# Optimization experiments

Measured on AMD Instinct MI355X. Metric: run time of the kernel, lower is better.

## Reference

```python
import jax, jax.numpy as jnp
import numpy as np

L = 6      # num encoder / decoder layers
H = 8      # num heads
D = 512    # dim_word
FF = 2048  # dim_feedforward
B = 8
S = 512


def _linear(x, W, b):
    return x @ W + b


def _mha(x_q, x_kv, W, b, num_heads):
    # W: [4, D, D] (q, k, v, out) stored as [in, out]; b: [4, D]
    Bb, Tq, Dd = x_q.shape
    Tk = x_kv.shape[1]
    dh = Dd // num_heads
    q = _linear(x_q, W[0], b[0]).reshape(Bb, Tq, num_heads, dh)
    k = _linear(x_kv, W[1], b[1]).reshape(Bb, Tk, num_heads, dh)
    v = _linear(x_kv, W[2], b[2]).reshape(Bb, Tk, num_heads, dh)
    # NOTE: original code divides by sqrt(dim_key_query_ALL_heads) == sqrt(D),
    # not sqrt(per-head dim) -- faithful to source.
    scores = jnp.einsum('bqhd,bkhd->bhqk', q, k) / jnp.sqrt(jnp.asarray(Dd, q.dtype))
    p = jax.nn.softmax(scores, axis=-1)
    z = jnp.einsum('bhqk,bkhd->bqhd', p, v).reshape(Bb, Tq, Dd)
    return _linear(z, W[3], b[3])


def _ln(z, alpha, beta):
    # Source uses torch .std() => unbiased (ddof=1), and NO epsilon.
    mean = jnp.mean(z, axis=-1, keepdims=True)
    std = jnp.std(z, axis=-1, ddof=1, keepdims=True)
    return (z - mean) / std * alpha + beta


def _ffn(x, W1, b1, W2, b2):
    return _linear(jax.nn.relu(_linear(x, W1, b1)), W2, b2)


def _forward(input_encoder, input_decoder, enc_W, enc_b, enc_W1, enc_b1,
             enc_W2, enc_b2, enc_alpha, enc_beta, dec_W, dec_b, dec_W1,
             dec_b1, dec_W2, dec_b2, dec_alpha, dec_beta, final_alpha,
             final_beta):
    z = input_encoder
    for i in range(L):
        a = _mha(z, z, enc_W[i], enc_b[i], H)
        z = _ln(a + z, enc_alpha[i, 0], enc_beta[i, 0])
        f = _ffn(z, enc_W1[i], enc_b1[i], enc_W2[i], enc_b2[i])
        z = _ln(z + f, enc_alpha[i, 1], enc_beta[i, 1])
    z_enc = _ln(z, final_alpha[0], final_beta[0])

    z = input_decoder
    for i in range(L):
        a = _mha(z, z, dec_W[i, 0], dec_b[i, 0], H)
        z1 = _ln(a + z, dec_alpha[i, 0], dec_beta[i, 0])
        c = _mha(z1, z_enc, dec_W[i, 1], dec_b[i, 1], H)
        z2 = _ln(c + z1, dec_alpha[i, 1], dec_beta[i, 1])
        f = _ffn(z2, dec_W1[i], dec_b1[i], dec_W2[i], dec_b2[i])
        z = _ln(z2 + f, dec_alpha[i, 2], dec_beta[i, 2])
    return _ln(z, final_alpha[1], final_beta[1])


def setup_inputs() -> dict:
    key = jax.random.key(0)
    ks = jax.random.split(key, 12)
    w_scale = 1.0 / np.sqrt(D)
    inp = {
        'input_encoder': jax.random.normal(ks[0], (B, S, D), jnp.float32),
        'input_decoder': jax.random.normal(ks[1], (B, S, D), jnp.float32),
        'enc_W': jax.random.normal(ks[2], (L, 4, D, D), jnp.float32) * w_scale,
        'enc_b': jnp.zeros((L, 4, D), jnp.float32),
        'enc_W1': jax.random.normal(ks[3], (L, D, FF), jnp.float32) * w_scale,
        'enc_b1': jnp.zeros((L, FF), jnp.float32),
        'enc_W2': jax.random.normal(ks[4], (L, FF, D), jnp.float32) * (1.0 / np.sqrt(FF)),
        'enc_b2': jnp.zeros((L, D), jnp.float32),
        'enc_alpha': jnp.ones((L, 2, D), jnp.float32),
        'enc_beta': jnp.zeros((L, 2, D), jnp.float32),
        'dec_W': jax.random.normal(ks[5], (L, 2, 4, D, D), jnp.float32) * w_scale,
        'dec_b': jnp.zeros((L, 2, 4, D), jnp.float32),
        'dec_W1': jax.random.normal(ks[6], (L, D, FF), jnp.float32) * w_scale,
        'dec_b1': jnp.zeros((L, FF), jnp.float32),
        'dec_W2': jax.random.normal(ks[7], (L, FF, D), jnp.float32) * (1.0 / np.sqrt(FF)),
        'dec_b2': jnp.zeros((L, D), jnp.float32),
        'dec_alpha': jnp.ones((L, 3, D), jnp.float32),
        'dec_beta': jnp.zeros((L, 3, D), jnp.float32),
        'final_alpha': jnp.ones((2, D), jnp.float32),
        'final_beta': jnp.zeros((2, D), jnp.float32),
    }
    return inp


def reference(input_encoder, input_decoder, enc_W, enc_b, enc_W1, enc_b1,
              enc_W2, enc_b2, enc_alpha, enc_beta, dec_W, dec_b, dec_W1,
              dec_b1, dec_W2, dec_b2, dec_alpha, dec_beta, final_alpha,
              final_beta):
    return _forward(input_encoder, input_decoder, enc_W, enc_b, enc_W1,
                    enc_b1, enc_W2, enc_b2, enc_alpha, enc_beta, dec_W,
                    dec_b, dec_W1, dec_b1, dec_W2, dec_b2, dec_alpha,
                    dec_beta, final_alpha, final_beta)
```

## Files before the change

### kernel.cpp

```cpp
#include <hip/hip_runtime.h>
#include <hip/hip_bf16.h>
#include <cstdint>

using bf16 = __hip_bfloat16;

typedef __bf16 bf16x8_t __attribute__((ext_vector_type(8)));
typedef float f32x4_t __attribute__((ext_vector_type(4)));
typedef unsigned short u16x8 __attribute__((ext_vector_type(8)));

enum { EPI_BF16 = 0, EPI_QKV = 2, EPI_RELU = 4 };

__device__ __forceinline__ unsigned short f2bf_bits(float f) {
    bf16 h = __float2bfloat16(f);
    return *reinterpret_cast<unsigned short*>(&h);
}
__device__ __forceinline__ float bfbits2f(unsigned short u) {
    return __uint_as_float(((unsigned)u) << 16);
}
__device__ __forceinline__ void gload16(const void* g, void* l) {
    __builtin_amdgcn_global_load_lds(
        (const __attribute__((address_space(1))) void*)g,
        (__attribute__((address_space(3))) void*)l, 16, 0, 0);
}

__global__ __launch_bounds__(256) void wtrans_kernel(
    const float* __restrict__ W, bf16* __restrict__ Wt, int Kd, int Nd) {
    __shared__ float tile[32][33];
    const int b = blockIdx.z;
    const float* Wb = W + (size_t)b * Kd * Nd;
    bf16* Tb = Wt + (size_t)b * Kd * Nd;
    const int n0 = blockIdx.x * 32, k0 = blockIdx.y * 32;
    const int tx = threadIdx.x, ty = threadIdx.y;
#pragma unroll
    for (int i = 0; i < 32; i += 8)
        tile[ty + i][tx] = Wb[(size_t)(k0 + ty + i) * Nd + n0 + tx];
    __syncthreads();
#pragma unroll
    for (int i = 0; i < 32; i += 8)
        Tb[(size_t)(n0 + ty + i) * Kd + k0 + tx] = __float2bfloat16(tile[tx][ty + i]);
}

__global__ __launch_bounds__(256) void dualcast_kernel(
    const float* __restrict__ x, float* __restrict__ of, bf16* __restrict__ ob) {
    const int i = blockIdx.x * 256 + threadIdx.x;
    float4 v = ((const float4*)x)[i];
    ((float4*)of)[i] = v;
    uint2 pk;
    pk.x = ((unsigned)f2bf_bits(v.y) << 16) | f2bf_bits(v.x);
    pk.y = ((unsigned)f2bf_bits(v.w) << 16) | f2bf_bits(v.z);
    ((uint2*)ob)[i] = pk;
}

template <int BM, int BN, int EPI, bool HASBIAS, int NT = 256, int WM = 2, int WN = 2>
__global__ __launch_bounds__(NT) void gemm_nt(
    const bf16* __restrict__ A, const bf16* __restrict__ B,
    const float* __restrict__ bias, void* __restrict__ Cout, void* __restrict__ Caux,
    int K, int ldA, int ldB, int ldC, int vcol0,
    long long oBz, long long oCz, long long oCvz, long long oBiasz) {
    static_assert(BM % 32 == 0 && BN % 32 == 0, "tile");
    static_assert(WM * WN == NT / 64, "wave grid");
    constexpr int RR = NT / 8;
    static_assert(BM % RR == 0 && BN % RR == 0, "staging");
    constexpr int WTM = (BM / WM) / 16;
    constexpr int WTN = (BN / WN) / 16;
    __shared__ alignas(16) bf16 lsA0[BM * 64];
    __shared__ alignas(16) bf16 lsB0[BN * 64];
    __shared__ alignas(16) bf16 lsA1[BM * 64];
    __shared__ alignas(16) bf16 lsB1[BN * 64];

    const int t = threadIdx.x;
    const int lane = t & 63;
    const int wave = t >> 6;
    const int wm = wave / WN, wn = wave % WN;
    const int z = blockIdx.z;

    const int brow = blockIdx.x * BM, bcol = blockIdx.y * BN;
    const bf16* Ab = A + (size_t)brow * ldA;
    const bf16* Bb = B + (long long)z * oBz + (size_t)bcol * ldB;
    const float* biasz = HASBIAS ? bias + (long long)z * oBiasz : bias;

    const int srow = t >> 3;
    const int sdst = (t & 7) * 8;
    const int ssrc = ((t & 7) ^ (srow & 7)) * 8;

    f32x4_t acc[WTM][WTN] = {};

#define GEMM_STAGE(AA, BB, kt)                                                \
    {                                                                         \
        _Pragma("unroll")                                                     \
        for (int r = 0; r < BM / RR; ++r)                                     \
            gload16(Ab + (size_t)(srow + r * RR) * ldA + (kt) + ssrc,         \
                    &AA[(srow + r * RR) * 64 + sdst]);                        \
        _Pragma("unroll")                                                     \
        for (int r = 0; r < BN / RR; ++r)                                     \
            gload16(Bb + (size_t)(srow + r * RR) * ldB + (kt) + ssrc,         \
                    &BB[(srow + r * RR) * 64 + sdst]);                        \
    }

#define GEMM_COMPUTE(AA, BB)                                                  \
    {                                                                         \
        _Pragma("unroll")                                                     \
        for (int ks = 0; ks < 2; ++ks) {                                      \
            bf16x8_t af[WTM], bfr[WTN];                                       \
            _Pragma("unroll")                                                 \
            for (int m = 0; m < WTM; ++m) {                                   \
                const int rowA = wm * (BM / WM) + m * 16 + (lane & 15);       \
                const int slot = ks * 4 + (lane >> 4);                        \
                af[m] = *(const bf16x8_t*)&AA[rowA * 64 + ((slot ^ (rowA & 7)) * 8)]; \
            }                                                                 \
            _Pragma("unroll")                                                 \
            for (int n = 0; n < WTN; ++n) {                                   \
                const int rowB = wn * (BN / WN) + n * 16 + (lane & 15);       \
                const int slot = ks * 4 + (lane >> 4);                        \
                bfr[n] = *(const bf16x8_t*)&BB[rowB * 64 + ((slot ^ (rowB & 7)) * 8)]; \
            }                                                                 \
            _Pragma("unroll")                                                 \
            for (int m = 0; m < WTM; ++m)                                     \
                _Pragma("unroll")                                             \
                for (int n = 0; n < WTN; ++n)                                 \
                    acc[m][n] = __builtin_amdgcn_mfma_f32_16x16x32_bf16(      \
                        af[m], bfr[n], acc[m][n], 0, 0, 0);                   \
        }                                                                     \
    }

    GEMM_STAGE(lsA0, lsB0, 0);
    __syncthreads();
    int kt = 0;
    while (true) {
        int kn = kt + 64;
        if (kn < K) GEMM_STAGE(lsA1, lsB1, kn);
        GEMM_COMPUTE(lsA0, lsB0);
        __syncthreads();
        kt = kn;
        if (kt >= K) break;
        kn = kt + 64;
        if (kn < K) GEMM_STAGE(lsA0, lsB0, kn);
        GEMM_COMPUTE(lsA1, lsB1);
        __syncthreads();
        kt = kn;
        if (kt >= K) break;
    }
#undef GEMM_STAGE
#undef GEMM_COMPUTE

    const int lr = (lane >> 4) * 4, lc = lane & 15;
#pragma unroll
    for (int m = 0; m < WTM; ++m) {
        const int gr0 = brow + wm * (BM / WM) + m * 16 + lr;
#pragma unroll
        for (int n = 0; n < WTN; ++n) {
            const int gc = bcol + wn * (BN / WN) + n * 16 + lc;
            float bv = 0.f;
            if constexpr (HASBIAS) bv = biasz[gc];
            float v[4];
#pragma unroll
            for (int r = 0; r < 4; ++r) {
                float x = acc[m][n][r] + bv;
                if constexpr (EPI == EPI_RELU) x = fmaxf(x, 0.f);
                v[r] = x;
            }
            if constexpr (EPI == EPI_QKV) {
                if (gc >= vcol0) {
                    bf16* Cv = (bf16*)Caux + (long long)z * oCvz;
                    const int bb = gr0 >> 9, q = gr0 & 511;
                    union { unsigned short h[4]; uint2 u; } pk;
#pragma unroll
                    for (int r = 0; r < 4; ++r) pk.h[r] = f2bf_bits(v[r]);
                    *(uint2*)&Cv[(size_t)bb * 262144 + (size_t)(gc - vcol0) * 512 + q] = pk.u;
                } else {
                    bf16* C = (bf16*)Cout + (long long)z * oCz;
#pragma unroll
                    for (int r = 0; r < 4; ++r)
                        C[(size_t)(gr0 + r) * ldC + gc] = __float2bfloat16(v[r]);
                }
            } else {
                bf16* C = (bf16*)Cout + (long long)z * oCz;
#pragma unroll
                for (int r = 0; r < 4; ++r)
                    C[(size_t)(gr0 + r) * ldC + gc] = __float2bfloat16(v[r]);
            }
        }
    }
}

__global__ __launch_bounds__(256) void flash_kernel(
    const bf16* __restrict__ Q, const bf16* __restrict__ Kg,
    const bf16* __restrict__ Vt, bf16* __restrict__ O,
    int ldK, int ldO, float qscale) {
    __shared__ alignas(16) bf16 klds[128 * 64];
    __shared__ alignas(16) bf16 vlds[64 * 128];
    __shared__ alignas(16) unsigned short plds[4][16 * 136];

    const int t = threadIdx.x, lane = t & 63, w = t >> 6;
    const int bh = blockIdx.x;
    const int b = bh >> 3, h = bh & 7;
    const int qb = blockIdx.y;

    const bf16* Qb = Q + (size_t)(b * 512 + qb * 64) * 1024 + h * 64;
    const bf16* Kb = Kg + (size_t)(b * 512) * ldK + h * 64;
    const bf16* Vb = Vt + (size_t)b * 262144 + (size_t)(h * 64) * 512;

    bf16x8_t qf[2];
    {
        const bf16* qr = Qb + (size_t)(w * 16 + (lane & 15)) * 1024 + (lane >> 4) * 8;
        qf[0] = *(const bf16x8_t*)qr;
        qf[1] = *(const bf16x8_t*)(qr + 32);
    }

    f32x4_t oacc[4] = {};
    float mrow[4] = {-1e30f, -1e30f, -1e30f, -1e30f};
    float lrow[4] = {0.f, 0.f, 0.f, 0.f};

    for (int kt = 0; kt < 4; ++kt) {
#pragma unroll
        for (int rd = 0; rd < 4; ++rd) {
            const int id = t + rd * 256;
            const int kr = id >> 3, sl = id & 7;
            gload16(Kb + (size_t)(kt * 128 + kr) * ldK + ((sl ^ (kr & 7)) * 8),
                    &klds[id * 8]);
        }
#pragma unroll
        for (int rd = 0; rd < 4; ++rd) {
            const int id = t + rd * 256;
            const int dr = id >> 4, sl = id & 15;
            gload16(Vb + (size_t)dr * 512 + kt * 128 + ((sl ^ (dr & 7)) * 8),
                    &vlds[id * 8]);
        }
        __syncthreads();

        f32x4_t sc[8] = {};
        __builtin_amdgcn_s_setprio(1);
#pragma unroll
        for (int kf = 0; kf < 8; ++kf) {
            const int krow = kf * 16 + (lane & 15);
#pragma unroll
            for (int ks = 0; ks < 2; ++ks) {
                const int slot = (ks * 4 + (lane >> 4)) ^ (krow & 7);
                bf16x8_t kfr = *(const bf16x8_t*)&klds[krow * 64 + slot * 8];
                sc[kf] = __builtin_amdgcn_mfma_f32_16x16x32_bf16(qf[ks], kfr, sc[kf], 0, 0, 0);
            }
        }
        __builtin_amdgcn_s_setprio(0);
        float tm[4] = {-1e30f, -1e30f, -1e30f, -1e30f};
#pragma unroll
        for (int kf = 0; kf < 8; ++kf)
#pragma unroll
            for (int r = 0; r < 4; ++r) {
                sc[kf][r] *= qscale;
                tm[r] = fmaxf(tm[r], sc[kf][r]);
            }
#pragma unroll
        for (int mm = 1; mm < 16; mm <<= 1)
#pragma unroll
            for (int r = 0; r < 4; ++r) tm[r] = fmaxf(tm[r], __shfl_xor(tm[r], mm, 64));
        float mnew[4], scal[4], ts[4] = {0.f, 0.f, 0.f, 0.f};
#pragma unroll
        for (int r = 0; r < 4; ++r) {
            mnew[r] = fmaxf(mrow[r], tm[r]);
            scal[r] = __expf(mrow[r] - mnew[r]);
            mrow[r] = mnew[r];
        }
#pragma unroll
        for (int kf = 0; kf < 8; ++kf)
#pragma unroll
            for (int r = 0; r < 4; ++r) {
                const float p = __expf(sc[kf][r] - mnew[r]);
                ts[r] += p;
                plds[w][((lane >> 4) * 4 + r) * 136 + kf * 16 + (lane & 15)] = f2bf_bits(p);
            }
#pragma unroll
        for (int mm = 1; mm < 16; mm <<= 1)
#pragma unroll
            for (int r = 0; r < 4; ++r) ts[r] += __shfl_xor(ts[r], mm, 64);
#pragma unroll
        for (int r = 0; r < 4; ++r) lrow[r] = lrow[r] * scal[r] + ts[r];
#pragma unroll
        for (int n = 0; n < 4; ++n)
#pragma unroll
            for (int r = 0; r < 4; ++r) oacc[n][r] *= scal[r];
        __builtin_amdgcn_s_setprio(1);
#pragma unroll
        for (int ks2 = 0; ks2 < 4; ++ks2) {
            bf16x8_t pa =
                *(const bf16x8_t*)&plds[w][(lane & 15) * 136 + ks2 * 32 + (lane >> 4) * 8];
#pragma unroll
            for (int n = 0; n < 4; ++n) {
                const int drow = n * 16 + (lane & 15);
                const int slot = (ks2 * 4 + (lane >> 4)) ^ (drow & 7);
                bf16x8_t vbf = *(const bf16x8_t*)&vlds[drow * 128 + slot * 8];
                oacc[n] = __builtin_amdgcn_mfma_f32_16x16x32_bf16(pa, vbf, oacc[n], 0, 0, 0);
            }
        }
        __builtin_amdgcn_s_setprio(0);
        __syncthreads();
    }
    bf16* Ob = O + (size_t)(b * 512 + qb * 64 + w * 16) * ldO + h * 64;
#pragma unroll
    for (int r = 0; r < 4; ++r) {
        const float inv = 1.0f / lrow[r];
        bf16* orow = Ob + (size_t)((lane >> 4) * 4 + r) * ldO;
#pragma unroll
        for (int n = 0; n < 4; ++n)
            orow[n * 16 + (lane & 15)] = __float2bfloat16(oacc[n][r] * inv);
    }
}

__global__ __launch_bounds__(256) void add_ln_kernel(
    const bf16* __restrict__ a, const float* __restrict__ x,
    const float* __restrict__ alpha, const float* __restrict__ beta,
    float* __restrict__ of, bf16* __restrict__ ob) {
    const int row = blockIdx.x * 4 + (threadIdx.x >> 6);
    const int lane = threadIdx.x & 63;
    const size_t base = (size_t)row * 512 + lane * 8;
    float v[8];
    {
        const float4* xp = (const float4*)(x + base);
        float4 x0 = xp[0], x1 = xp[1];
        v[0] = x0.x; v[1] = x0.y; v[2] = x0.z; v[3] = x0.w;
        v[4] = x1.x; v[5] = x1.y; v[6] = x1.z; v[7] = x1.w;
    }
    if (a) {
        u16x8 u = *(const u16x8*)(a + base);
#pragma unroll
        for (int j = 0; j < 8; ++j) v[j] += bfbits2f(u[j]);
    }
    float s = 0.f, ss = 0.f;
#pragma unroll
    for (int j = 0; j < 8; ++j) { s += v[j]; ss += v[j] * v[j]; }
#pragma unroll
    for (int m = 1; m < 64; m <<= 1) {
        s += __shfl_xor(s, m, 64);
        ss += __shfl_xor(ss, m, 64);
    }
    const float mean = s * (1.0f / 512.0f);
    const float var = (ss - s * mean) * (1.0f / 511.0f);
    const float rstd = rsqrtf(var);
    const int col = lane * 8;
    const float4* alp = (const float4*)(alpha + col);
    const float4* bep = (const float4*)(beta + col);
    float4 al0 = alp[0], al1 = alp[1], be0 = bep[0], be1 = bep[1];
    float al[8] = {al0.x, al0.y, al0.z, al0.w, al1.x, al1.y, al1.z, al1.w};
    float be[8] = {be0.x, be0.y, be0.z, be0.w, be1.x, be1.y, be1.z, be1.w};
    float y[8];
#pragma unroll
    for (int j = 0; j < 8; ++j) y[j] = (v[j] - mean) * rstd * al[j] + be[j];
    if (of) {
        float4 o0, o1;
        o0.x = y[0]; o0.y = y[1]; o0.z = y[2]; o0.w = y[3];
        o1.x = y[4]; o1.y = y[5]; o1.z = y[6]; o1.w = y[7];
        float4* op = (float4*)(of + base);
        op[0] = o0; op[1] = o1;
    }
    if (ob) {
        u16x8 u;
#pragma unroll
        for (int j = 0; j < 8; ++j) u[j] = f2bf_bits(y[j]);
        *(u16x8*)(ob + base) = u;
    }
}

extern "C" void kernel_launch(void* const* d_in, const int* in_sizes, int n_in,
                              void* d_out, int out_size, void* d_ws, size_t ws_size,
                              hipStream_t stream) {
    (void)in_sizes; (void)n_in; (void)out_size;

    const float* in_enc = (const float*)d_in[0];
    const float* in_dec = (const float*)d_in[1];
    const float* enc_W  = (const float*)d_in[2];
    const float* enc_b  = (const float*)d_in[3];
    const float* enc_W1 = (const float*)d_in[4];
    const float* enc_b1 = (const float*)d_in[5];
    const float* enc_W2 = (const float*)d_in[6];
    const float* enc_b2 = (const float*)d_in[7];
    const float* enc_al = (const float*)d_in[8];
    const float* enc_be = (const float*)d_in[9];
    const float* dec_W  = (const float*)d_in[10];
    const float* dec_b  = (const float*)d_in[11];
    const float* dec_W1 = (const float*)d_in[12];
    const float* dec_b1 = (const float*)d_in[13];
    const float* dec_W2 = (const float*)d_in[14];
    const float* dec_b2 = (const float*)d_in[15];
    const float* dec_al = (const float*)d_in[16];
    const float* dec_be = (const float*)d_in[17];
    const float* fin_al = (const float*)d_in[18];
    const float* fin_be = (const float*)d_in[19];

    constexpr int Dm = 512, FFm = 2048, Lm = 6;
    constexpr int M = 4096;
    const size_t DD = (size_t)Dm * Dm;
    const size_t DFF = (size_t)Dm * FFm;
    const long long MD = (long long)M * Dm;
    const float QSCALE = 0.04419417382415922f;

    char* wsp = (char*)d_ws;
    auto alloc = [&](size_t bytes) -> char* {
        char* p = wsp;
        wsp += (bytes + 255) & ~(size_t)255;
        return p;
    };

    bf16* wtEncW  = (bf16*)alloc(sizeof(bf16) * 24 * DD);
    bf16* wtEncW1 = (bf16*)alloc(sizeof(bf16) * 6 * DFF);
    bf16* wtEncW2 = (bf16*)alloc(sizeof(bf16) * 6 * DFF);
    bf16* wtDecW  = (bf16*)alloc(sizeof(bf16) * 48 * DD);
    bf16* wtDecW1 = (bf16*)alloc(sizeof(bf16) * 6 * DFF);
    bf16* wtDecW2 = (bf16*)alloc(sizeof(bf16) * 6 * DFF);
    bf16* qkvbuf = (bf16*)alloc(sizeof(bf16) * M * 1024);
    bf16* vt     = (bf16*)alloc(sizeof(bf16) * M * Dm);
    bf16* ckbuf  = (bf16*)alloc(sizeof(bf16) * M * Dm);
    bf16* ck6    = (bf16*)alloc(sizeof(bf16) * 6 * M * Dm);
    bf16* cv6    = (bf16*)alloc(sizeof(bf16) * 6 * M * Dm);
    bf16* ffnmid = (bf16*)alloc(sizeof(bf16) * M * FFm);
    bf16* projb  = (bf16*)alloc(sizeof(bf16) * M * Dm);
    float* zAf = (float*)alloc(sizeof(float) * M * Dm);
    bf16*  zAb = (bf16*)alloc(sizeof(bf16) * M * Dm);
    float* zBf = (float*)alloc(sizeof(float) * M * Dm);
    bf16*  zBb = (bf16*)alloc(sizeof(bf16) * M * Dm);
    bf16*  zencb = (bf16*)alloc(sizeof(bf16) * M * Dm);

    if ((size_t)(wsp - (char*)d_ws) > ws_size) return;

    {
        dim3 bl(32, 8);
        wtrans_kernel<<<dim3(Dm / 32, Dm / 32, 24), bl, 0, stream>>>(enc_W, wtEncW, Dm, Dm);
        wtrans_kernel<<<dim3(FFm / 32, Dm / 32, 6), bl, 0, stream>>>(enc_W1, wtEncW1, Dm, FFm);
        wtrans_kernel<<<dim3(Dm / 32, FFm / 32, 6), bl, 0, stream>>>(enc_W2, wtEncW2, FFm, Dm);
        wtrans_kernel<<<dim3(Dm / 32, Dm / 32, 48), bl, 0, stream>>>(dec_W, wtDecW, Dm, Dm);
        wtrans_kernel<<<dim3(FFm / 32, Dm / 32, 6), bl, 0, stream>>>(dec_W1, wtDecW1, Dm, FFm);
        wtrans_kernel<<<dim3(Dm / 32, FFm / 32, 6), bl, 0, stream>>>(dec_W2, wtDecW2, FFm, Dm);
    }

    float* curF = zAf; bf16* curB = zAb;
    float* othF = zBf; bf16* othB = zBb;
    auto swapbuf = [&]() {
        float* tf = curF; curF = othF; othF = tf;
        bf16* tb = curB; curB = othB; othB = tb;
    };

    auto self_attention = [&](const bf16* src, const bf16* Wt4, const float* b4) {
        gemm_nt<128, 128, EPI_QKV, true, 512, 2, 4><<<dim3(32, 12, 1), 512, 0, stream>>>(
            src, Wt4, b4, qkvbuf, vt, Dm, Dm, Dm, 1024, 1024, 0, 0, 0, 0);
        flash_kernel<<<dim3(64, 8), 256, 0, stream>>>(
            qkvbuf, qkvbuf + 512, vt, ckbuf, 1024, 512, QSCALE);
        gemm_nt<64, 64, EPI_BF16, true, 256, 2, 2><<<dim3(64, 8, 1), 256, 0, stream>>>(
            ckbuf, Wt4 + 3 * DD, b4 + 3 * Dm, projb, nullptr, Dm, 512, Dm, Dm, 0,
            0, 0, 0, 0);
    };

    auto cross_attention = [&](const bf16* src, const bf16* Wt4, const float* b4, int i) {
        gemm_nt<64, 64, EPI_BF16, true, 256, 2, 2><<<dim3(64, 8, 1), 256, 0, stream>>>(
            src, Wt4, b4, qkvbuf, nullptr, Dm, Dm, Dm, 1024, 0, 0, 0, 0, 0);
        flash_kernel<<<dim3(64, 8), 256, 0, stream>>>(
            qkvbuf, ck6 + (long long)i * MD, cv6 + (long long)i * MD, qkvbuf + 512,
            512, 1024, QSCALE);
        gemm_nt<64, 64, EPI_BF16, true, 256, 2, 2><<<dim3(64, 8, 1), 256, 0, stream>>>(
            qkvbuf + 512, Wt4 + 3 * DD, b4 + 3 * Dm, projb, nullptr, Dm, 1024, Dm, Dm, 0,
            0, 0, 0, 0);
    };

    auto ffn = [&](const bf16* src, const bf16* W1t, const float* b1v,
                   const bf16* W2t, const float* b2v) {
        gemm_nt<128, 128, EPI_RELU, true, 512, 2, 4><<<dim3(32, 16, 1), 512, 0, stream>>>(
            src, W1t, b1v, ffnmid, nullptr, Dm, Dm, Dm, FFm, 0, 0, 0, 0, 0);
        gemm_nt<64, 64, EPI_BF16, true, 256, 2, 2><<<dim3(64, 8, 1), 256, 0, stream>>>(
            ffnmid, W2t, b2v, projb, nullptr, FFm, FFm, FFm, Dm, 0, 0, 0, 0, 0);
    };

    dualcast_kernel<<<2048, 256, 0, stream>>>(in_enc, curF, curB);
    for (int i = 0; i < Lm; ++i) {
        self_attention(curB, wtEncW + (size_t)i * 4 * DD, enc_b + (size_t)i * 4 * Dm);
        add_ln_kernel<<<1024, 256, 0, stream>>>(
            projb, curF, enc_al + (size_t)(i * 2) * Dm, enc_be + (size_t)(i * 2) * Dm,
            othF, othB);
        swapbuf();
        ffn(curB, wtEncW1 + (size_t)i * DFF, enc_b1 + (size_t)i * FFm,
            wtEncW2 + (size_t)i * DFF, enc_b2 + (size_t)i * Dm);
        add_ln_kernel<<<1024, 256, 0, stream>>>(
            projb, curF, enc_al + (size_t)(i * 2 + 1) * Dm, enc_be + (size_t)(i * 2 + 1) * Dm,
            othF, othB);
        swapbuf();
    }
    add_ln_kernel<<<1024, 256, 0, stream>>>(nullptr, curF, fin_al, fin_be, nullptr, zencb);

    gemm_nt<128, 128, EPI_QKV, true, 512, 2, 4><<<dim3(32, 8, 6), 512, 0, stream>>>(
        zencb, wtDecW + 5 * DD, dec_b + 5 * Dm, ck6, cv6, Dm, Dm, Dm, 512, 512,
        8LL * (long long)DD, MD, MD, 8LL * Dm);

    curF = zAf; curB = zAb; othF = zBf; othB = zBb;
    dualcast_kernel<<<2048, 256, 0, stream>>>(in_dec, curF, curB);
    for (int i = 0; i < Lm; ++i) {
        self_attention(curB, wtDecW + (size_t)(i * 2 + 0) * 4 * DD,
                       dec_b + (size_t)(i * 2 + 0) * 4 * Dm);
        add_ln_kernel<<<1024, 256, 0, stream>>>(
            projb, curF, dec_al + (size_t)(i * 3 + 0) * Dm, dec_be + (size_t)(i * 3 + 0) * Dm,
            othF, othB);
        swapbuf();
        cross_attention(curB, wtDecW + (size_t)(i * 2 + 1) * 4 * DD,
                        dec_b + (size_t)(i * 2 + 1) * 4 * Dm, i);
        add_ln_kernel<<<1024, 256, 0, stream>>>(
            projb, curF, dec_al + (size_t)(i * 3 + 1) * Dm, dec_be + (size_t)(i * 3 + 1) * Dm,
            othF, othB);
        swapbuf();
        ffn(curB, wtDecW1 + (size_t)i * DFF, dec_b1 + (size_t)i * FFm,
            wtDecW2 + (size_t)i * DFF, dec_b2 + (size_t)i * Dm);
        add_ln_kernel<<<1024, 256, 0, stream>>>(
            projb, curF, dec_al + (size_t)(i * 3 + 2) * Dm, dec_be + (size_t)(i * 3 + 2) * Dm,
            othF, othB);
        swapbuf();
    }
    add_ln_kernel<<<1024, 256, 0, stream>>>(nullptr, curF, fin_al + Dm, fin_be + Dm,
                                            (float*)d_out, nullptr);
}
```

Before: 1.325 ms.

## Stage GEMM and attention outputs through LDS and drop fp32 residual stream

GEMM epilogues now write their tiles into a swizzled LDS buffer that aliases the staging buffers, then issue coalesced 16-byte global stores. The V-transpose path gets the same treatment, and the flash kernel output is also staged in LDS. The fp32 residual copies are removed, so add+LayerNorm reads the bf16 residual and writes only bf16. This cuts global traffic and uncoalesced stores, at the cost of an extra barrier and reduced precision on the residual stream.

Measured after the change: 1.217 ms. -8.1%, faster.

```diff
diff --git a/kernel.cpp b/kernel.cpp
--- a/kernel.cpp
+++ b/kernel.cpp
@@ -40,11 +40,10 @@
         Tb[(size_t)(n0 + ty + i) * Kd + k0 + tx] = __float2bfloat16(tile[tx][ty + i]);
 }
 
-__global__ __launch_bounds__(256) void dualcast_kernel(
-    const float* __restrict__ x, float* __restrict__ of, bf16* __restrict__ ob) {
+__global__ __launch_bounds__(256) void cast_kernel(
+    const float* __restrict__ x, bf16* __restrict__ ob) {
     const int i = blockIdx.x * 256 + threadIdx.x;
     float4 v = ((const float4*)x)[i];
-    ((float4*)of)[i] = v;
     uint2 pk;
     pk.x = ((unsigned)f2bf_bits(v.y) << 16) | f2bf_bits(v.x);
     pk.y = ((unsigned)f2bf_bits(v.w) << 16) | f2bf_bits(v.z);
@@ -63,10 +62,13 @@
     static_assert(BM % RR == 0 && BN % RR == 0, "staging");
     constexpr int WTM = (BM / WM) / 16;
     constexpr int WTN = (BN / WN) / 16;
-    __shared__ alignas(16) bf16 lsA0[BM * 64];
-    __shared__ alignas(16) bf16 lsB0[BN * 64];
-    __shared__ alignas(16) bf16 lsA1[BM * 64];
-    __shared__ alignas(16) bf16 lsB1[BN * 64];
+    constexpr int STG = 2 * (BM + BN) * 64;
+    constexpr int CTE = BM * BN;
+    __shared__ alignas(16) bf16 smem[STG > CTE ? STG : CTE];
+    bf16* lsA0 = smem;
+    bf16* lsB0 = smem + BM * 64;
+    bf16* lsA1 = smem + (BM + BN) * 64;
+    bf16* lsB1 = lsA1 + BM * 64;
 
     const int t = threadIdx.x;
     const int lane = t & 63;
@@ -144,41 +146,50 @@
 #undef GEMM_COMPUTE
 
     const int lr = (lane >> 4) * 4, lc = lane & 15;
+    const bool isV = (EPI == EPI_QKV) && (bcol >= vcol0);
+    unsigned short* cts = (unsigned short*)smem;
 #pragma unroll
     for (int m = 0; m < WTM; ++m) {
-        const int gr0 = brow + wm * (BM / WM) + m * 16 + lr;
+        const int row0 = wm * (BM / WM) + m * 16 + lr;
 #pragma unroll
         for (int n = 0; n < WTN; ++n) {
-            const int gc = bcol + wn * (BN / WN) + n * 16 + lc;
+            const int col = wn * (BN / WN) + n * 16 + lc;
             float bv = 0.f;
-            if constexpr (HASBIAS) bv = biasz[gc];
-            float v[4];
+            if constexpr (HASBIAS) bv = biasz[bcol + col];
+            unsigned short h4[4];
 #pragma unroll
             for (int r = 0; r < 4; ++r) {
                 float x = acc[m][n][r] + bv;
                 if constexpr (EPI == EPI_RELU) x = fmaxf(x, 0.f);
-                v[r] = x;
+                h4[r] = f2bf_bits(x);
             }
-            if constexpr (EPI == EPI_QKV) {
-                if (gc >= vcol0) {
-                    bf16* Cv = (bf16*)Caux + (long long)z * oCvz;
-                    const int bb = gr0 >> 9, q = gr0 & 511;
-                    union { unsigned short h[4]; uint2 u; } pk;
-#pragma unroll
-                    for (int r = 0; r < 4; ++r) pk.h[r] = f2bf_bits(v[r]);
-                    *(uint2*)&Cv[(size_t)bb * 262144 + (size_t)(gc - vcol0) * 512 + q] = pk.u;
-                } else {
-                    bf16* C = (bf16*)Cout + (long long)z * oCz;
-#pragma unroll
-                    for (int r = 0; r < 4; ++r)
-                        C[(size_t)(gr0 + r) * ldC + gc] = __float2bfloat16(v[r]);
-                }
+            if (isV) {
+                union { unsigned short h[4]; uint2 u; } pk;
+#pragma unroll
+                for (int r = 0; r < 4; ++r) pk.h[r] = h4[r];
+                *(uint2*)&cts[col * BM + (row0 ^ ((col & 7) << 3))] = pk.u;
             } else {
-                bf16* C = (bf16*)Cout + (long long)z * oCz;
 #pragma unroll
                 for (int r = 0; r < 4; ++r)
-                    C[(size_t)(gr0 + r) * ldC + gc] = __float2bfloat16(v[r]);
+                    cts[(row0 + r) * BN + (col ^ (((row0 + r) & 7) << 3))] = h4[r];
             }
+        }
+    }
+    __syncthreads();
+    if (isV) {
+        bf16* Cv = (bf16*)Caux + (long long)z * oCvz;
+        const int bb = brow >> 9, qb0 = brow & 511;
+        for (int s = t; s < CTE / 8; s += NT) {
+            const int d = s / (BM / 8), q8 = (s % (BM / 8)) * 8;
+            u16x8 val = *(const u16x8*)&cts[d * BM + (q8 ^ ((d & 7) << 3))];
+            *(u16x8*)&Cv[(size_t)bb * 262144 + (size_t)(bcol - vcol0 + d) * 512 + qb0 + q8] = val;
+        }
+    } else {
+        bf16* C = (bf16*)Cout + (long long)z * oCz;
+        for (int s = t; s < CTE / 8; s += NT) {
+            const int row = s / (BN / 8), c8 = (s % (BN / 8)) * 8;
+            u16x8 val = *(const u16x8*)&cts[row * BN + (c8 ^ ((row & 7) << 3))];
+            *(u16x8*)&C[(size_t)(brow + row) * ldC + bcol + c8] = val;
         }
     }
 }
@@ -294,19 +305,29 @@
         __builtin_amdgcn_s_setprio(0);
         __syncthreads();
     }
-    bf16* Ob = O + (size_t)(b * 512 + qb * 64 + w * 16) * ldO + h * 64;
 #pragma unroll
     for (int r = 0; r < 4; ++r) {
         const float inv = 1.0f / lrow[r];
-        bf16* orow = Ob + (size_t)((lane >> 4) * 4 + r) * ldO;
 #pragma unroll
         for (int n = 0; n < 4; ++n)
-            orow[n * 16 + (lane & 15)] = __float2bfloat16(oacc[n][r] * inv);
+            plds[w][((lane >> 4) * 4 + r) * 136 + n * 16 + (lane & 15)] =
+                f2bf_bits(oacc[n][r] * inv);
+    }
+    __syncthreads();
+    {
+        bf16* Ob = O + (size_t)(b * 512 + qb * 64 + w * 16) * ldO + h * 64;
+#pragma unroll
+        for (int it = 0; it < 2; ++it) {
+            const int seg = lane + it * 64;
+            const int row = seg >> 3, c8 = (seg & 7) * 8;
+            u16x8 val = *(const u16x8*)&plds[w][row * 136 + c8];
+            *(u16x8*)&Ob[(size_t)row * ldO + c8] = val;
+        }
     }
 }
 
 __global__ __launch_bounds__(256) void add_ln_kernel(
-    const bf16* __restrict__ a, const float* __restrict__ x,
+    const bf16* __restrict__ a, const bf16* __restrict__ x,
     const float* __restrict__ alpha, const float* __restrict__ beta,
     float* __restrict__ of, bf16* __restrict__ ob) {
     const int row = blockIdx.x * 4 + (threadIdx.x >> 6);
@@ -314,15 +335,14 @@
     const size_t base = (size_t)row * 512 + lane * 8;
     float v[8];
     {
-        const float4* xp = (const float4*)(x + base);
-        float4 x0 = xp[0], x1 = xp[1];
-        v[0] = x0.x; v[1] = x0.y; v[2] = x0.z; v[3] = x0.w;
-        v[4] = x1.x; v[5] = x1.y; v[6] = x1.z; v[7] = x1.w;
+        u16x8 ux = *(const u16x8*)(x + base);
+#pragma unroll
+        for (int j = 0; j < 8; ++j) v[j] = bfbits2f(ux[j]);
     }
     if (a) {
-        u16x8 u = *(const u16x8*)(a + base);
-#pragma unroll
-        for (int j = 0; j < 8; ++j) v[j] += bfbits2f(u[j]);
+        u16x8 ua = *(const u16x8*)(a + base);
+#pragma unroll
+        for (int j = 0; j < 8; ++j) v[j] += bfbits2f(ua[j]);
     }
     float s = 0.f, ss = 0.f;
 #pragma unroll
@@ -344,18 +364,18 @@
     float y[8];
 #pragma unroll
     for (int j = 0; j < 8; ++j) y[j] = (v[j] - mean) * rstd * al[j] + be[j];
+    if (ob) {
+        u16x8 u;
+#pragma unroll
+        for (int j = 0; j < 8; ++j) u[j] = f2bf_bits(y[j]);
+        *(u16x8*)(ob + base) = u;
+    }
     if (of) {
         float4 o0, o1;
         o0.x = y[0]; o0.y = y[1]; o0.z = y[2]; o0.w = y[3];
         o1.x = y[4]; o1.y = y[5]; o1.z = y[6]; o1.w = y[7];
         float4* op = (float4*)(of + base);
         op[0] = o0; op[1] = o1;
-    }
-    if (ob) {
-        u16x8 u;
-#pragma unroll
-        for (int j = 0; j < 8; ++j) u[j] = f2bf_bits(y[j]);
-        *(u16x8*)(ob + base) = u;
     }
 }
 
@@ -412,11 +432,9 @@
     bf16* cv6    = (bf16*)alloc(sizeof(bf16) * 6 * M * Dm);
     bf16* ffnmid = (bf16*)alloc(sizeof(bf16) * M * FFm);
     bf16* projb  = (bf16*)alloc(sizeof(bf16) * M * Dm);
-    float* zAf = (float*)alloc(sizeof(float) * M * Dm);
-    bf16*  zAb = (bf16*)alloc(sizeof(bf16) * M * Dm);
-    float* zBf = (float*)alloc(sizeof(float) * M * Dm);
-    bf16*  zBb = (bf16*)alloc(sizeof(bf16) * M * Dm);
-    bf16*  zencb = (bf16*)alloc(sizeof(bf16) * M * Dm);
+    bf16* zAb = (bf16*)alloc(sizeof(bf16) * M * Dm);
+    bf16* zBb = (bf16*)alloc(sizeof(bf16) * M * Dm);
+    bf16* zencb = (bf16*)alloc(sizeof(bf16) * M * Dm);
 
     if ((size_t)(wsp - (char*)d_ws) > ws_size) return;
 
@@ -430,12 +448,9 @@
         wtrans_kernel<<<dim3(Dm / 32, FFm / 32, 6), bl, 0, stream>>>(dec_W2, wtDecW2, FFm, Dm);
     }
 
-    float* curF = zAf; bf16* curB = zAb;
-    float* othF = zBf; bf16* othB = zBb;
-    auto swapbuf = [&]() {
-        float* tf = curF; curF = othF; othF = tf;
-        bf16* tb = curB; curB = othB; othB = tb;
-    };
+    bf16* curB = zAb;
+    bf16* othB = zBb;
+    auto swapbuf = [&]() { bf16* tb = curB; curB = othB; othB = tb; };
 
     auto self_attention = [&](const bf16* src, const bf16* Wt4, const float* b4) {
         gemm_nt<128, 128, EPI_QKV, true, 512, 2, 4><<<dim3(32, 12, 1), 512, 0, stream>>>(
@@ -466,48 +481,48 @@
             ffnmid, W2t, b2v, projb, nullptr, FFm, FFm, FFm, Dm, 0, 0, 0, 0, 0);
     };
 
-    dualcast_kernel<<<2048, 256, 0, stream>>>(in_enc, curF, curB);
+    cast_kernel<<<2048, 256, 0, stream>>>(in_enc, curB);
     for (int i = 0; i < Lm; ++i) {
         self_attention(curB, wtEncW + (size_t)i * 4 * DD, enc_b + (size_t)i * 4 * Dm);
         add_ln_kernel<<<1024, 256, 0, stream>>>(
-            projb, curF, enc_al + (size_t)(i * 2) * Dm, enc_be + (size_t)(i * 2) * Dm,
-            othF, othB);
+            projb, curB, enc_al + (size_t)(i * 2) * Dm, enc_be + (size_t)(i * 2) * Dm,
+            nullptr, othB);
         swapbuf();
         ffn(curB, wtEncW1 + (size_t)i * DFF, enc_b1 + (size_t)i * FFm,
             wtEncW2 + (size_t)i * DFF, enc_b2 + (size_t)i * Dm);
         add_ln_kernel<<<1024, 256, 0, stream>>>(
-            projb, curF, enc_al + (size_t)(i * 2 + 1) * Dm, enc_be + (size_t)(i * 2 + 1) * Dm,
-            othF, othB);
+            projb, curB, enc_al + (size_t)(i * 2 + 1) * Dm, enc_be + (size_t)(i * 2 + 1) * Dm,
+            nullptr, othB);
         swapbuf();
     }
-    add_ln_kernel<<<1024, 256, 0, stream>>>(nullptr, curF, fin_al, fin_be, nullptr, zencb);
+    add_ln_kernel<<<1024, 256, 0, stream>>>(nullptr, curB, fin_al, fin_be, nullptr, zencb);
 
     gemm_nt<128, 128, EPI_QKV, true, 512, 2, 4><<<dim3(32, 8, 6), 512, 0, stream>>>(
         zencb, wtDecW + 5 * DD, dec_b + 5 * Dm, ck6, cv6, Dm, Dm, Dm, 512, 512,
         8LL * (long long)DD, MD, MD, 8LL * Dm);
 
-    curF = zAf; curB = zAb; othF = zBf; othB = zBb;
-    dualcast_kernel<<<2048, 256, 0, stream>>>(in_dec, curF, curB);
+    curB = zAb; othB = zBb;
+    cast_kernel<<<2048, 256, 0, stream>>>(in_dec, curB);
     for (int i = 0; i < Lm; ++i) {
         self_attention(curB, wtDecW + (size_t)(i * 2 + 0) * 4 * DD,
                        dec_b + (size_t)(i * 2 + 0) * 4 * Dm);
         add_ln_kernel<<<1024, 256, 0, stream>>>(
-            projb, curF, dec_al + (size_t)(i * 3 + 0) * Dm, dec_be + (size_t)(i * 3 + 0) * Dm,
-            othF, othB);
+            projb, curB, dec_al + (size_t)(i * 3 + 0) * Dm, dec_be + (size_t)(i * 3 + 0) * Dm,
+            nullptr, othB);
         swapbuf();
         cross_attention(curB, wtDecW + (size_t)(i * 2 + 1) * 4 * DD,
                         dec_b + (size_t)(i * 2 + 1) * 4 * Dm, i);
         add_ln_kernel<<<1024, 256, 0, stream>>>(
-            projb, curF, dec_al + (size_t)(i * 3 + 1) * Dm, dec_be + (size_t)(i * 3 + 1) * Dm,
-            othF, othB);
+            projb, curB, dec_al + (size_t)(i * 3 + 1) * Dm, dec_be + (size_t)(i * 3 + 1) * Dm,
+            nullptr, othB);
         swapbuf();
         ffn(curB, wtDecW1 + (size_t)i * DFF, dec_b1 + (size_t)i * FFm,
             wtDecW2 + (size_t)i * DFF, dec_b2 + (size_t)i * Dm);
         add_ln_kernel<<<1024, 256, 0, stream>>>(
-            projb, curF, dec_al + (size_t)(i * 3 + 2) * Dm, dec_be + (size_t)(i * 3 + 2) * Dm,
-            othF, othB);
+            projb, curB, dec_al + (size_t)(i * 3 + 2) * Dm, dec_be + (size_t)(i * 3 + 2) * Dm,
+            nullptr, othB);
         swapbuf();
     }
-    add_ln_kernel<<<1024, 256, 0, stream>>>(nullptr, curF, fin_al + Dm, fin_be + Dm,
+    add_ln_kernel<<<1024, 256, 0, stream>>>(nullptr, curB, fin_al + Dm, fin_be + Dm,
                                             (float*)d_out, nullptr);
 }
```
